# Optimization experiments

Measured on AMD Instinct MI355X. Metric: run time of the kernel, lower is better.

The kernel has to match this reference:

```python
import jax, jax.numpy as jnp
import numpy as np

D_MODEL = 1024
H = 16          # n_heads (kv heads)
G = 2           # n_gqa_groups
DQ = 64         # d_queries
DV = 64         # d_values
MAXLEN = 2048
NSEG = 8
SEG = MAXLEN // NSEG  # 256
EPS = 1e-5
ROPE_THETA = 10000.0


def setup_inputs() -> dict:
    key = jax.random.key(0)
    ks = jax.random.split(key, 10)
    N = 8
    w = lambda k, sh: jax.random.normal(k, sh, dtype=jnp.float32) * 0.02
    return {
        "query_sequences": jax.random.normal(ks[0], (N, MAXLEN, D_MODEL), dtype=jnp.float32),
        "key_sequences": jax.random.normal(ks[1], (N, MAXLEN, D_MODEL), dtype=jnp.float32),
        "value_sequences": jax.random.normal(ks[2], (N, MAXLEN, D_MODEL), dtype=jnp.float32),
        "ln_w": jnp.ones((D_MODEL,), dtype=jnp.float32),
        "ln_b": jnp.zeros((D_MODEL,), dtype=jnp.float32),
        "Wq": w(ks[3], (G * H * DQ, D_MODEL)),
        "Wk": w(ks[4], (H * DQ, D_MODEL)),
        "Wv": w(ks[5], (H * DV, D_MODEL)),
        "Wo": w(ks[6], (D_MODEL, H * DV)),
        "Wkc": w(ks[7], (DQ, SEG * DQ)),
        "bkc": jnp.zeros((DQ,), dtype=jnp.float32),
        "Wvc": w(ks[8], (DV, SEG * DV)),
        "bvc": jnp.zeros((DV,), dtype=jnp.float32),
    }


def _layernorm(x, w, b):
    mu = x.mean(-1, keepdims=True)
    var = ((x - mu) ** 2).mean(-1, keepdims=True)
    return (x - mu) * jax.lax.rsqrt(var + EPS) * w + b


def _rope(x):
    # x: [..., seq, DQ]; full-dim interleaved RoPE (rotary-embedding-torch convention)
    seq = x.shape[-2]
    inv_freq = 1.0 / (ROPE_THETA ** (jnp.arange(0, DQ, 2, dtype=jnp.float32) / DQ))  # [DQ/2]
    ang = jnp.arange(seq, dtype=jnp.float32)[:, None] * inv_freq[None, :]            # [seq, DQ/2]
    ang = jnp.repeat(ang, 2, axis=-1)                                                # [seq, DQ]
    cos, sin = jnp.cos(ang), jnp.sin(ang)
    x2 = x.reshape(x.shape[:-1] + (DQ // 2, 2))
    xrot = jnp.stack([-x2[..., 1], x2[..., 0]], axis=-1).reshape(x.shape)
    return x * cos + xrot * sin


def _forward(query_sequences, key_sequences, value_sequences,
             ln_w, ln_b, Wq, Wk, Wv, Wo, Wkc, bkc, Wvc, bvc):
    N, t, _ = query_sequences.shape
    q = _layernorm(query_sequences, ln_w, ln_b)
    k = _layernorm(key_sequences, ln_w, ln_b)
    v = _layernorm(value_sequences, ln_w, ln_b)

    qh = (q @ Wq.T).reshape(N, t, G, H, DQ).transpose(0, 2, 3, 1, 4)  # [N,G,H,t,DQ]
    kh = (k @ Wk.T).reshape(N, t, H, DQ).transpose(0, 2, 1, 3)        # [N,H,T,DQ]
    vh = (v @ Wv.T).reshape(N, t, H, DV).transpose(0, 2, 1, 3)        # [N,H,T,DV]

    qh = _rope(qh)
    kh = _rope(kh)

    # split into NSEG segments along time; keep last 2 raw, compress the rest
    kseg = kh.reshape(N, H, NSEG, SEG, DQ)
    vseg = vh.reshape(N, H, NSEG, SEG, DV)
    recent_k = kseg[:, :, -2:].reshape(N, H, 2 * SEG, DQ)
    recent_v = vseg[:, :, -2:].reshape(N, H, 2 * SEG, DV)
    k_sum = jax.nn.elu(kseg[:, :, :-2].reshape(N, H, NSEG - 2, SEG * DQ) @ Wkc.T + bkc)  # [N,H,S-2,DQ]
    v_sum = jax.nn.elu(vseg[:, :, :-2].reshape(N, H, NSEG - 2, SEG * DV) @ Wvc.T + bvc)
    K = jnp.concatenate([k_sum, recent_k], axis=-2)  # [N,H,Tk,DQ], Tk = (NSEG-2) + 2*SEG
    V = jnp.concatenate([v_sum, recent_v], axis=-2)

    # NOTE: original einsum sums over the GQA group axis g
    attn = jnp.einsum('nghtq,nhTq->nhtT', qh, K) * (1.0 / DQ ** 0.5)
    attn = 30.0 * jnp.tanh(attn / 30.0)  # grok scaled attn

    Tk = K.shape[-2]
    causal = jnp.arange(Tk)[None, :] <= jnp.arange(t)[:, None]  # tril slice [t, Tk]
    attn = jnp.where(causal, attn, -jnp.inf)
    attn = jax.nn.softmax(attn, axis=-1)

    out = jnp.einsum('nhtT,nhTv->nhtv', attn, V)
    out = out.transpose(0, 2, 1, 3).reshape(N, t, H * DV)
    return out @ Wo.T


def reference(query_sequences, key_sequences, value_sequences,
              ln_w, ln_b, Wq, Wk, Wv, Wo, Wkc, bkc, Wvc, bvc):
    return _forward(query_sequences, key_sequences, value_sequences,
                    ln_w, ln_b, Wq, Wk, Wv, Wo, Wkc, bkc, Wvc, bvc)
```

## Files before the change

### kernel.cpp

```cpp
#include <hip/hip_runtime.h>
#include <stdint.h>

#define DEV static __device__ __forceinline__

typedef unsigned short u16;
typedef unsigned int u32;
typedef __attribute__((ext_vector_type(4))) float f32x4;
typedef __attribute__((ext_vector_type(8))) short bf16x8;

DEV float bf2f(u16 u) { u32 x = ((u32)u) << 16; float f; __builtin_memcpy(&f, &x, 4); return f; }
DEV u16 f2bf(float f) { u32 x; __builtin_memcpy(&x, &f, 4); x = x + 0x7fffu + ((x >> 16) & 1u); return (u16)(x >> 16); }
DEV float lo16(u32 p) { u32 x = p << 16; float f; __builtin_memcpy(&f, &x, 4); return f; }
DEV float hi16(u32 p) { u32 x = p & 0xffff0000u; float f; __builtin_memcpy(&f, &x, 4); return f; }
DEV u32 pack2(float a, float b) { return (u32)f2bf(a) | ((u32)f2bf(b) << 16); }

DEV u32 cvtpk(float lo, float hi) {
  u32 r; asm("v_cvt_pk_bf16_f32 %0, %1, %2" : "=v"(r) : "v"(lo), "v"(hi)); return r;
}
DEV bf16x8 pk8(f32x4 a, f32x4 b) {
  union { u32 u[4]; bf16x8 v; } x;
  x.u[0] = cvtpk(a[0], a[1]); x.u[1] = cvtpk(a[2], a[3]);
  x.u[2] = cvtpk(b[0], b[1]); x.u[3] = cvtpk(b[2], b[3]);
  return x.v;
}

DEV f32x4 mfma16(bf16x8 a, bf16x8 b, f32x4 c) {
  return __builtin_amdgcn_mfma_f32_16x16x32_bf16(a, b, c, 0, 0, 0);
}

DEV void gl_lds16(const u16* g, u16* l) {
  __builtin_amdgcn_global_load_lds((const __attribute__((address_space(1))) void*)g,
                                   (__attribute__((address_space(3))) void*)l, 16, 0, 0);
}

__global__ __launch_bounds__(256) void prep_wqe_kernel(const float* __restrict__ Wq, u16* __restrict__ out) {
  int id = blockIdx.x * 256 + threadIdx.x;
  float4 a = ((const float4*)Wq)[id];
  float4 b = ((const float4*)Wq)[id + 262144];
  ushort4 o; o.x = f2bf(a.x + b.x); o.y = f2bf(a.y + b.y); o.z = f2bf(a.z + b.z); o.w = f2bf(a.w + b.w);
  ((ushort4*)out)[id] = o;
}

__global__ __launch_bounds__(256) void cast_w_kernel(const float* __restrict__ src, u16* __restrict__ dst) {
  int id = blockIdx.x * 256 + threadIdx.x;
  float4 a = ((const float4*)src)[id];
  ushort4 o; o.x = f2bf(a.x); o.y = f2bf(a.y); o.z = f2bf(a.z); o.w = f2bf(a.w);
  ((ushort4*)dst)[id] = o;
}

__global__ __launch_bounds__(256) void rope_cs_kernel(float* __restrict__ cs) {
  int id = blockIdx.x * 256 + threadIdx.x;
  int t = id >> 5, i = id & 31;
  double ang = (double)t * pow(10000.0, -(double)(2 * i) / 64.0);
  cs[id * 2] = (float)cos(ang);
  cs[id * 2 + 1] = (float)sin(ang);
}

__global__ __launch_bounds__(256) void ln_kernel(const float* __restrict__ x, const float* __restrict__ w,
                                                 const float* __restrict__ b, u16* __restrict__ out) {
  int row = blockIdx.x, t = threadIdx.x;
  float4 v = ((const float4*)(x + (size_t)row * 1024))[t];
  float s = v.x + v.y + v.z + v.w;
  float s2 = v.x * v.x + v.y * v.y + v.z * v.z + v.w * v.w;
#pragma unroll
  for (int off = 32; off; off >>= 1) { s += __shfl_xor(s, off, 64); s2 += __shfl_xor(s2, off, 64); }
  __shared__ float red[8];
  if ((t & 63) == 0) { red[t >> 6] = s; red[4 + (t >> 6)] = s2; }
  __syncthreads();
  s = red[0] + red[1] + red[2] + red[3];
  s2 = red[4] + red[5] + red[6] + red[7];
  float mu = s * 0.0009765625f;
  float var = s2 * 0.0009765625f - mu * mu;
  float rstd = rsqrtf(var + 1e-5f);
  float4 wv = ((const float4*)w)[t];
  float4 bv = ((const float4*)b)[t];
  ushort4 o;
  o.x = f2bf((v.x - mu) * rstd * wv.x + bv.x);
  o.y = f2bf((v.y - mu) * rstd * wv.y + bv.y);
  o.z = f2bf((v.z - mu) * rstd * wv.z + bv.z);
  o.w = f2bf((v.w - mu) * rstd * wv.w + bv.w);
  *(ushort4*)(out + (size_t)row * 1024 + t * 4) = o;
}

template <int MODE>
__global__ __launch_bounds__(256, 2) void gemm_nt(const u16* __restrict__ A, const u16* __restrict__ B,
                                                  void* __restrict__ Cout, int M, int Nd, int K,
                                                  const float* __restrict__ cs) {
  __shared__ u16 As[4096], Bs[4096];
  int tid = threadIdx.x, lane = tid & 63, wv = tid >> 6;
  int l15 = lane & 15, lq = lane >> 4;
  int bm = blockIdx.x * 128, bn = blockIdx.y * 128;
  int wm = (wv >> 1) * 64, wn = (wv & 1) * 64;
  f32x4 acc[4][4] = {};
  for (int k0 = 0; k0 < K; k0 += 32) {
    __syncthreads();
#pragma unroll
    for (int it = 0; it < 2; ++it) {
      int ia = wv * 2 + it;
      int row = ia * 16 + (lane >> 2);
      int qs = lane & 3;
      int qg = qs ^ (row & 3);
      gl_lds16(A + (size_t)(bm + row) * K + k0 + qg * 8, &As[ia * 512]);
      gl_lds16(B + (size_t)(bn + row) * K + k0 + qg * 8, &Bs[ia * 512]);
    }
    __syncthreads();
    bf16x8 af[4], bfr[4];
#pragma unroll
    for (int mt = 0; mt < 4; ++mt) {
      int r = wm + mt * 16 + l15;
      af[mt] = *(const bf16x8*)&As[r * 32 + ((lq ^ (r & 3)) * 8)];
    }
#pragma unroll
    for (int nt = 0; nt < 4; ++nt) {
      int r = wn + nt * 16 + l15;
      bfr[nt] = *(const bf16x8*)&Bs[r * 32 + ((lq ^ (r & 3)) * 8)];
    }
#pragma unroll
    for (int mt = 0; mt < 4; ++mt)
#pragma unroll
      for (int nt = 0; nt < 4; ++nt)
        acc[mt][nt] = mfma16(af[mt], bfr[nt], acc[mt][nt]);
  }
#pragma unroll
  for (int mt = 0; mt < 4; ++mt)
#pragma unroll
    for (int nt = 0; nt < 4; ++nt)
#pragma unroll
      for (int i = 0; i < 4; ++i) {
        int row = bm + wm + mt * 16 + lq * 4 + i;
        int col = bn + wn + nt * 16 + l15;
        float x = acc[mt][nt][i];
        if (MODE == 1) {
          ((float*)Cout)[(size_t)row * Nd + col] = x;
        } else if (MODE == 0) {
          ((u16*)Cout)[(size_t)row * Nd + col] = f2bf(x);
        } else {
          float xp = __shfl_xor(x, 1, 64);
          int t = row & 2047;
          int i0 = (col & 63) >> 1;
          float2 csv = *(const float2*)(cs + ((size_t)t * 32 + i0) * 2);
          float r = (col & 1) ? (x * csv.x + xp * csv.y) : (x * csv.x - xp * csv.y);
          ((u16*)Cout)[(size_t)row * Nd + col] = f2bf(r);
        }
      }
}

__global__ __launch_bounds__(512) void compress_partial_kernel(
    const u16* __restrict__ kh, const u16* __restrict__ vh,
    const u16* __restrict__ wkcb, const u16* __restrict__ wvcb,
    float* __restrict__ part) {
  int mt = blockIdx.x, ksl = blockIdx.y, kv = blockIdx.z;
  const u16* src = kv ? vh : kh;
  const u16* W = kv ? wvcb : wkcb;
  int tid = threadIdx.x, lane = tid & 63, wv = tid >> 6;
  int l15 = lane & 15, lq = lane >> 4;
  int r = mt * 16 + l15;
  int nh = r / 6, s = r % 6;
  int n = nh >> 4, h = nh & 15;
  const u16* arow = src + ((size_t)(n * 2048 + s * 256)) * 1024 + h * 64;
  f32x4 acc[4] = {};
  int kbase = (ksl * 8 + wv) * 256;
#pragma unroll
  for (int ks = 0; ks < 8; ++ks) {
    int k0 = kbase + ks * 32;
    int tau = k0 >> 6, d0 = k0 & 63;
    bf16x8 a = *(const bf16x8*)(arow + (size_t)tau * 1024 + d0 + lq * 8);
#pragma unroll
    for (int nt = 0; nt < 4; ++nt) {
      bf16x8 b = *(const bf16x8*)(W + (size_t)(nt * 16 + l15) * 16384 + k0 + lq * 8);
      acc[nt] = mfma16(a, b, acc[nt]);
    }
  }
  __shared__ float red[8][16][68];
#pragma unroll
  for (int nt = 0; nt < 4; ++nt)
#pragma unroll
    for (int i = 0; i < 4; ++i)
      red[wv][lq * 4 + i][nt * 16 + l15] = acc[nt][i];
  __syncthreads();
  int row = tid >> 5, o0 = (tid & 31) * 2;
  float v0 = 0.f, v1 = 0.f;
#pragma unroll
  for (int w8 = 0; w8 < 8; ++w8) { v0 += red[w8][row][o0]; v1 += red[w8][row][o0 + 1]; }
  size_t base = ((size_t)(kv * 8 + ksl) * 768 + mt * 16 + row) * 64 + o0;
  part[base] = v0;
  part[base + 1] = v1;
}

__global__ __launch_bounds__(256) void compress_finalize_kernel(
    const float* __restrict__ part, const float* __restrict__ bkc, const float* __restrict__ bvc,
    u16* __restrict__ kp, u16* __restrict__ vtp) {
  int id = blockIdx.x * 256 + threadIdx.x;
  int kv = blockIdx.y;
  int r = id >> 6, o = id & 63;
  float v = kv ? bvc[o] : bkc[o];
#pragma unroll
  for (int s8 = 0; s8 < 8; ++s8) v += part[((size_t)(kv * 8 + s8) * 768 + r) * 64 + o];
  v = v > 0.f ? v : expm1f(v);
  int nh = r / 6, s = r % 6;
  if (kv) vtp[((size_t)nh * 64 + o) * 576 + s] = f2bf(v);
  else    kp[((size_t)nh * 576 + s) * 64 + o] = f2bf(v);
}

__global__ __launch_bounds__(256) void copy_recent_kernel(const u16* __restrict__ kh, const u16* __restrict__ vh,
                                                          u16* __restrict__ kp, u16* __restrict__ vtp) {
  int bid = blockIdx.x;
  if (bid < 2280) {
    int u = bid * 256 + threadIdx.x;
    int dq8 = u & 7; int rest = u >> 3; int Tm6 = rest % 570; int nh = rest / 570;
    if (nh >= 128) return;
    uint4 val = {0, 0, 0, 0};
    if (Tm6 < 512) {
      int n = nh >> 4, h = nh & 15;
      val = *(const uint4*)&kh[((size_t)(n * 2048 + 1536 + Tm6)) * 1024 + h * 64 + dq8 * 8];
    }
    *(uint4*)&kp[((size_t)nh * 576 + 6 + Tm6) * 64 + dq8 * 8] = val;
  } else {
    int u = (bid - 2280) * 256 + threadIdx.x;
    int d = u & 63; int rest = u >> 6; int tch = rest % 72; int nh = rest / 72;
    if (nh >= 128) return;
    int n = nh >> 4, h = nh & 15;
#pragma unroll
    for (int ii = 0; ii < 8; ++ii) {
      int T = tch * 8 + ii;
      if (T < 6) continue;
      u16 v = 0;
      if (T < 518) v = vh[((size_t)(n * 2048 + 1536 + (T - 6))) * 1024 + h * 64 + d];
      vtp[((size_t)nh * 64 + d) * 576 + T] = v;
    }
  }
}

__global__ __launch_bounds__(256) void attn_kernel(const u16* __restrict__ qc, const u16* __restrict__ Kp,
                                                   const u16* __restrict__ VTp, u16* __restrict__ ao) {
  int qt = blockIdx.x, h = blockIdx.y, n = blockIdx.z;
  int tid = threadIdx.x, lane = tid & 63, wv = tid >> 6;
  int l15 = lane & 15, lq = lane >> 4;
  __shared__ u16 KS[4096], VS[4096];
  __shared__ float PS[4][1088];
  int q0 = qt * 64 + wv * 16;
  const u16* qrowp = qc + ((size_t)(n * 2048 + q0 + l15)) * 1024 + h * 64;
  bf16x8 aq0 = *(const bf16x8*)(qrowp + lq * 8);
  bf16x8 aq1 = *(const bf16x8*)(qrowp + 32 + lq * 8);
  const u16* Kph = Kp + (size_t)(n * 16 + h) * 576 * 64;
  const u16* Vph = VTp + (size_t)(n * 16 + h) * 64 * 576;
  f32x4 oa[4] = {};
  float rs[4] = {0.f, 0.f, 0.f, 0.f};
  float* PSW = &PS[wv][0];
  const float C1 = 0.012022458674074693f;
  const float C2 = -86.56170245333781f;
  int nchunks = min(qt + 1, 9);
  int srow0 = tid >> 3, sq0 = tid & 7;
  int srow1 = (256 + tid) >> 3, sq1 = tid & 7;
  int ksw0 = srow0 * 64 + ((sq0 ^ (srow0 & 7)) * 8);
  int ksw1 = srow1 * 64 + ((sq1 ^ (srow1 & 7)) * 8);
  uint4 kr0, kr1, vr0, vr1;
  {
    kr0 = *(const uint4*)&Kph[(size_t)srow0 * 64 + sq0 * 8];
    kr1 = *(const uint4*)&Kph[(size_t)srow1 * 64 + sq1 * 8];
    vr0 = *(const uint4*)&Vph[(size_t)srow0 * 576 + sq0 * 8];
    vr1 = *(const uint4*)&Vph[(size_t)srow1 * 576 + sq1 * 8];
  }
  for (int tc = 0; tc < nchunks; ++tc) {
    __syncthreads();
    *(uint4*)&KS[ksw0] = kr0;
    *(uint4*)&KS[ksw1] = kr1;
    *(uint4*)&VS[ksw0] = vr0;
    *(uint4*)&VS[ksw1] = vr1;
    if (tc + 1 < nchunks) {
      int Tb = (tc + 1) * 64;
      kr0 = *(const uint4*)&Kph[(size_t)(Tb + srow0) * 64 + sq0 * 8];
      kr1 = *(const uint4*)&Kph[(size_t)(Tb + srow1) * 64 + sq1 * 8];
      vr0 = *(const uint4*)&Vph[(size_t)srow0 * 576 + Tb + sq0 * 8];
      vr1 = *(const uint4*)&Vph[(size_t)srow1 * 576 + Tb + sq1 * 8];
    }
    __syncthreads();
    f32x4 sv[4];
    __builtin_amdgcn_s_setprio(1);
#pragma unroll
    for (int tt = 0; tt < 4; ++tt) {
      int row = tt * 16 + l15, r7 = row & 7;
      bf16x8 b0 = *(const bf16x8*)&KS[row * 64 + ((lq ^ r7) * 8)];
      bf16x8 b1 = *(const bf16x8*)&KS[row * 64 + (((4 | lq) ^ r7) * 8)];
      f32x4 c = {0.f, 0.f, 0.f, 0.f};
      c = mfma16(aq0, b0, c);
      c = mfma16(aq1, b1, c);
      sv[tt] = c;
    }
    __builtin_amdgcn_s_setprio(0);
    float p[4][4];
    bool needmask = (tc == qt) || (tc == 8);
    if (needmask) {
      int qb = q0 + lq * 4;
      int Tbase = tc * 64;
#pragma unroll
      for (int tt = 0; tt < 4; ++tt) {
        int T = Tbase + tt * 16 + l15;
        bool tval = (T < 518);
#pragma unroll
        for (int i = 0; i < 4; ++i) {
          float e = __builtin_amdgcn_exp2f(sv[tt][i] * C1);
          float pe = __builtin_amdgcn_exp2f(C2 * __builtin_amdgcn_rcpf(e + 1.f));
          bool ok = tval && (T <= qb + i);
          pe = ok ? pe : 0.f;
          p[tt][i] = pe;
          rs[i] += pe;
        }
      }
    } else {
#pragma unroll
      for (int tt = 0; tt < 4; ++tt)
#pragma unroll
        for (int i = 0; i < 4; ++i) {
          float e = __builtin_amdgcn_exp2f(sv[tt][i] * C1);
          float pe = __builtin_amdgcn_exp2f(C2 * __builtin_amdgcn_rcpf(e + 1.f));
          p[tt][i] = pe;
          rs[i] += pe;
        }
    }
#pragma unroll
    for (int tt = 0; tt < 4; ++tt)
#pragma unroll
      for (int i = 0; i < 4; ++i)
        PSW[(lq * 4 + i) * 68 + tt * 16 + l15] = p[tt][i];
    const float* prow = PSW + l15 * 68;
    f32x4 r0a = *(const f32x4*)(prow + lq * 8);
    f32x4 r0b = *(const f32x4*)(prow + lq * 8 + 4);
    f32x4 r1a = *(const f32x4*)(prow + lq * 8 + 32);
    f32x4 r1b = *(const f32x4*)(prow + lq * 8 + 36);
    bf16x8 pa0 = pk8(r0a, r0b);
    bf16x8 pa1 = pk8(r1a, r1b);
    __builtin_amdgcn_s_setprio(1);
#pragma unroll
    for (int ct = 0; ct < 4; ++ct) {
      int row = ct * 16 + l15, r7 = row & 7;
      bf16x8 bv0 = *(const bf16x8*)&VS[row * 64 + ((lq ^ r7) * 8)];
      bf16x8 bv1 = *(const bf16x8*)&VS[row * 64 + (((4 | lq) ^ r7) * 8)];
      oa[ct] = mfma16(pa0, bv0, oa[ct]);
      oa[ct] = mfma16(pa1, bv1, oa[ct]);
    }
    __builtin_amdgcn_s_setprio(0);
  }
#pragma unroll
  for (int i = 0; i < 4; ++i)
#pragma unroll
    for (int off = 1; off < 16; off <<= 1) rs[i] += __shfl_xor(rs[i], off, 64);
  u16* aop = ao + ((size_t)(n * 2048)) * 1024 + h * 64;
#pragma unroll
  for (int i = 0; i < 4; ++i) {
    float inv = 1.0f / rs[i];
    int q = q0 + lq * 4 + i;
#pragma unroll
    for (int ct = 0; ct < 4; ++ct) {
      int dv = ct * 16 + l15;
      aop[(size_t)q * 1024 + dv] = f2bf(oa[ct][i] * inv);
    }
  }
}

extern "C" void kernel_launch(void* const* d_in, const int* in_sizes, int n_in,
                              void* d_out, int out_size, void* d_ws, size_t ws_size,
                              hipStream_t stream) {
  const float* q_in = (const float*)d_in[0];
  const float* k_in = (const float*)d_in[1];
  const float* v_in = (const float*)d_in[2];
  const float* ln_w = (const float*)d_in[3];
  const float* ln_b = (const float*)d_in[4];
  const float* Wq = (const float*)d_in[5];
  const float* Wk = (const float*)d_in[6];
  const float* Wv = (const float*)d_in[7];
  const float* Wo = (const float*)d_in[8];
  const float* Wkc = (const float*)d_in[9];
  const float* bkc = (const float*)d_in[10];
  const float* Wvc = (const float*)d_in[11];
  const float* bvc = (const float*)d_in[12];

  char* ws = (char*)d_ws;
  const size_t MB = 1u << 20;
  u16* wqe = (u16*)(ws + 0 * MB);
  u16* wkb = (u16*)(ws + 2 * MB);
  u16* wvb = (u16*)(ws + 4 * MB);
  u16* wob = (u16*)(ws + 6 * MB);
  u16* wkcb = (u16*)(ws + 8 * MB);
  u16* wvcb = (u16*)(ws + 10 * MB);
  float* csb = (float*)(ws + 12 * MB);
  u16* xn = (u16*)(ws + 13 * MB);
  float* partf = (float*)(ws + 13 * MB);
  u16* qcb = (u16*)(ws + 45 * MB);
  u16* khb = (u16*)(ws + 77 * MB);
  u16* vhb = (u16*)(ws + 109 * MB);
  u16* kp = (u16*)(ws + 141 * MB);
  u16* vtp = (u16*)(ws + 141 * MB + 9437184);
  u16* aob = khb;

  prep_wqe_kernel<<<1024, 256, 0, stream>>>(Wq, wqe);
  cast_w_kernel<<<1024, 256, 0, stream>>>(Wk, wkb);
  cast_w_kernel<<<1024, 256, 0, stream>>>(Wv, wvb);
  cast_w_kernel<<<1024, 256, 0, stream>>>(Wo, wob);
  cast_w_kernel<<<1024, 256, 0, stream>>>(Wkc, wkcb);
  cast_w_kernel<<<1024, 256, 0, stream>>>(Wvc, wvcb);
  rope_cs_kernel<<<256, 256, 0, stream>>>(csb);

  dim3 gg(128, 8);
  ln_kernel<<<16384, 256, 0, stream>>>(q_in, ln_w, ln_b, xn);
  gemm_nt<2><<<gg, 256, 0, stream>>>(xn, wqe, qcb, 16384, 1024, 1024, csb);
  ln_kernel<<<16384, 256, 0, stream>>>(k_in, ln_w, ln_b, xn);
  gemm_nt<2><<<gg, 256, 0, stream>>>(xn, wkb, khb, 16384, 1024, 1024, csb);
  ln_kernel<<<16384, 256, 0, stream>>>(v_in, ln_w, ln_b, xn);
  gemm_nt<0><<<gg, 256, 0, stream>>>(xn, wvb, vhb, 16384, 1024, 1024, csb);

  compress_partial_kernel<<<dim3(48, 8, 2), 512, 0, stream>>>(khb, vhb, wkcb, wvcb, partf);
  compress_finalize_kernel<<<dim3(192, 2), 256, 0, stream>>>(partf, bkc, bvc, kp, vtp);
  copy_recent_kernel<<<4584, 256, 0, stream>>>(khb, vhb, kp, vtp);
  attn_kernel<<<dim3(32, 16, 8), 256, 0, stream>>>(qcb, kp, vtp, aob);
  gemm_nt<1><<<gg, 256, 0, stream>>>(aob, wob, (float*)d_out, 16384, 1024, 1024, csb);
}
```

Measured before the change: 435.1 us.

## Load K/V MFMA fragments directly from global memory, drop LDS staging

The attention kernel no longer stages K and V chunks through shared memory with register prefetch and two block barriers per chunk. Each wave now loads its MFMA B-operand fragments straight from global memory (relying on L1/L2, since all four waves read the same K/V). It also drops the setprio hints and adds a min-blocks-per-SM hint of 6 to raise occupancy. The trade is more global/cache traffic and exposed load latency in exchange for removing LDS writes and barriers.

```diff
diff --git a/kernel.cpp b/kernel.cpp
--- a/kernel.cpp
+++ b/kernel.cpp
@@ -231,12 +231,11 @@
   }
 }
 
-__global__ __launch_bounds__(256) void attn_kernel(const u16* __restrict__ qc, const u16* __restrict__ Kp,
-                                                   const u16* __restrict__ VTp, u16* __restrict__ ao) {
+__global__ __launch_bounds__(256, 6) void attn_kernel(const u16* __restrict__ qc, const u16* __restrict__ Kp,
+                                                      const u16* __restrict__ VTp, u16* __restrict__ ao) {
   int qt = blockIdx.x, h = blockIdx.y, n = blockIdx.z;
   int tid = threadIdx.x, lane = tid & 63, wv = tid >> 6;
   int l15 = lane & 15, lq = lane >> 4;
-  __shared__ u16 KS[4096], VS[4096];
   __shared__ float PS[4][1088];
   int q0 = qt * 64 + wv * 16;
   const u16* qrowp = qc + ((size_t)(n * 2048 + q0 + l15)) * 1024 + h * 64;
@@ -250,49 +249,27 @@
   const float C1 = 0.012022458674074693f;
   const float C2 = -86.56170245333781f;
   int nchunks = min(qt + 1, 9);
-  int srow0 = tid >> 3, sq0 = tid & 7;
-  int srow1 = (256 + tid) >> 3, sq1 = tid & 7;
-  int ksw0 = srow0 * 64 + ((sq0 ^ (srow0 & 7)) * 8);
-  int ksw1 = srow1 * 64 + ((sq1 ^ (srow1 & 7)) * 8);
-  uint4 kr0, kr1, vr0, vr1;
-  {
-    kr0 = *(const uint4*)&Kph[(size_t)srow0 * 64 + sq0 * 8];
-    kr1 = *(const uint4*)&Kph[(size_t)srow1 * 64 + sq1 * 8];
-    vr0 = *(const uint4*)&Vph[(size_t)srow0 * 576 + sq0 * 8];
-    vr1 = *(const uint4*)&Vph[(size_t)srow1 * 576 + sq1 * 8];
-  }
+  const u16* kfp0 = Kph + (size_t)l15 * 64 + lq * 8;
+  const u16* kfp1 = Kph + (size_t)l15 * 64 + (4 | lq) * 8;
+  const u16* vfp0 = Vph + (size_t)l15 * 576 + lq * 8;
+  const u16* vfp1 = Vph + (size_t)l15 * 576 + (4 | lq) * 8;
   for (int tc = 0; tc < nchunks; ++tc) {
-    __syncthreads();
-    *(uint4*)&KS[ksw0] = kr0;
-    *(uint4*)&KS[ksw1] = kr1;
-    *(uint4*)&VS[ksw0] = vr0;
-    *(uint4*)&VS[ksw1] = vr1;
-    if (tc + 1 < nchunks) {
-      int Tb = (tc + 1) * 64;
-      kr0 = *(const uint4*)&Kph[(size_t)(Tb + srow0) * 64 + sq0 * 8];
-      kr1 = *(const uint4*)&Kph[(size_t)(Tb + srow1) * 64 + sq1 * 8];
-      vr0 = *(const uint4*)&Vph[(size_t)srow0 * 576 + Tb + sq0 * 8];
-      vr1 = *(const uint4*)&Vph[(size_t)srow1 * 576 + Tb + sq1 * 8];
-    }
-    __syncthreads();
+    int Tbase = tc * 64;
     f32x4 sv[4];
-    __builtin_amdgcn_s_setprio(1);
 #pragma unroll
     for (int tt = 0; tt < 4; ++tt) {
-      int row = tt * 16 + l15, r7 = row & 7;
-      bf16x8 b0 = *(const bf16x8*)&KS[row * 64 + ((lq ^ r7) * 8)];
-      bf16x8 b1 = *(const bf16x8*)&KS[row * 64 + (((4 | lq) ^ r7) * 8)];
+      size_t ro = (size_t)(Tbase + tt * 16) * 64;
+      bf16x8 b0 = *(const bf16x8*)(kfp0 + ro);
+      bf16x8 b1 = *(const bf16x8*)(kfp1 + ro);
       f32x4 c = {0.f, 0.f, 0.f, 0.f};
       c = mfma16(aq0, b0, c);
       c = mfma16(aq1, b1, c);
       sv[tt] = c;
     }
-    __builtin_amdgcn_s_setprio(0);
     float p[4][4];
     bool needmask = (tc == qt) || (tc == 8);
     if (needmask) {
       int qb = q0 + lq * 4;
-      int Tbase = tc * 64;
 #pragma unroll
       for (int tt = 0; tt < 4; ++tt) {
         int T = Tbase + tt * 16 + l15;
@@ -330,16 +307,14 @@
     f32x4 r1b = *(const f32x4*)(prow + lq * 8 + 36);
     bf16x8 pa0 = pk8(r0a, r0b);
     bf16x8 pa1 = pk8(r1a, r1b);
-    __builtin_amdgcn_s_setprio(1);
 #pragma unroll
     for (int ct = 0; ct < 4; ++ct) {
-      int row = ct * 16 + l15, r7 = row & 7;
-      bf16x8 bv0 = *(const bf16x8*)&VS[row * 64 + ((lq ^ r7) * 8)];
-      bf16x8 bv1 = *(const bf16x8*)&VS[row * 64 + (((4 | lq) ^ r7) * 8)];
+      size_t co = (size_t)(ct * 16) * 576 + Tbase;
+      bf16x8 bv0 = *(const bf16x8*)(vfp0 + co);
+      bf16x8 bv1 = *(const bf16x8*)(vfp1 + co);
       oa[ct] = mfma16(pa0, bv0, oa[ct]);
       oa[ct] = mfma16(pa1, bv1, oa[ct]);
     }
-    __builtin_amdgcn_s_setprio(0);
   }
 #pragma unroll
   for (int i = 0; i < 4; ++i)
```

Measured after the change: 613.3 us. +40.9%, slower.
